# Performance work log

Hardware: AMD Instinct MI355X
Metric: run time of the kernel (lower is better)

## Reference

```python
import jax, jax.numpy as jnp
import numpy as np

KSIZE = 3   # patch kernel
NSIZE = 7   # search neighborhood
SCALE = 4   # downscale factor
ALPHA = 1


def _patches(x, k, pad_mode):
    # x: [b,c,h,w] -> [b, c*k*k, h, w], feature ordering channel-major
    # (matches torch.nn.functional.unfold ordering).
    if pad_mode == 'reflect':
        p = k // 2
        xp = jnp.pad(x, ((0, 0), (0, 0), (p, p), (p, p)), mode='reflect')
        return jax.lax.conv_general_dilated_patches(xp, (k, k), (1, 1), 'VALID')
    return jax.lax.conv_general_dilated_patches(x, (k, k), (1, 1), 'SAME')


def census(x):
    # UFlow-style soft census transform (the CensusTransform used in this repo):
    # grayscale*255, 3x3 zero-padded patches minus center, soft-sign normalize.
    gray = (0.299 * x[:, 0:1] + 0.587 * x[:, 1:2] + 0.114 * x[:, 2:3]) * 255.0
    p = _patches(gray, KSIZE, 'zero')          # [b, 9, h, w]
    t = p - gray
    return t / jnp.sqrt(0.81 + t * t)


def downsample(x):
    b, c, h, w = x.shape
    return jax.image.resize(x, (b, c, h // SCALE, w // SCALE), method='cubic')


def unfold_center(x):
    # _unfold(data, with_unfold=False): [b,c,h,w] -> [b, hw, c*k*k]
    x = downsample(x)
    b, c, h, w = x.shape
    p = _patches(x, KSIZE, 'reflect').reshape(b, c * KSIZE * KSIZE, h * w)
    return p.transpose(0, 2, 1)


def unfold_nbr(x):
    # _unfold(data, with_unfold=True): [b,c,h,w] -> [b, hw, n*n, c*k*k]
    x = downsample(x)
    b, c, h, w = x.shape
    d1 = _patches(x, KSIZE, 'reflect')          # [b, c*k*k, h, w]
    c1 = d1.shape[1]
    d2 = _patches(d1, NSIZE, 'reflect')         # [b, c1*n*n, h, w]
    d2 = d2.reshape(b, c1, NSIZE * NSIZE, h * w)
    return d2.transpose(0, 3, 2, 1)


def reference(pred, I):
    # --- census-space distance + argmin over 2*n*n candidates ---
    p_ct = unfold_center(census(pred))                       # [b, hw, 81]
    nbr_ct = jnp.concatenate(
        [unfold_nbr(census(I[:, 0])), unfold_nbr(census(I[:, 1]))], axis=2
    )                                                        # [b, hw, 2n^2, 81]
    # ||p - n||^2 expanded as p2 + n2 - 2 p.n (avoids the huge repeated diff)
    p2 = jnp.sum(p_ct * p_ct, axis=-1)                       # [b, hw]
    n2 = jnp.sum(nbr_ct * nbr_ct, axis=-1)                   # [b, hw, 2n^2]
    dis = p2[:, :, None] + n2 - 2.0 * jnp.einsum('bpc,bpnc->bpn', p_ct, nbr_ct)
    ind = jnp.argmin(dis, axis=2)                            # [b, hw]
    # --- gather matched raw patches and compute loss ---
    p = unfold_center(pred)                                  # [b, hw, 27]
    nbr = jnp.concatenate(
        [unfold_nbr(I[:, 0]), unfold_nbr(I[:, 1])], axis=2
    )                                                        # [b, hw, 2n^2, 27]
    matched = jnp.take_along_axis(nbr, ind[:, :, None, None], axis=2)[:, :, 0]
    return jnp.mean((p - matched) ** 2 * 0.5)


def setup_inputs() -> dict:
    key = jax.random.key(0)
    k1, k2 = jax.random.split(key)
    pred = jax.random.normal(k1, (2, 3, 384, 384), dtype=jnp.float32)
    I = jax.random.normal(k2, (2, 2, 3, 384, 384), dtype=jnp.float32)
    return {'pred': pred, 'I': I}
```

## Files before the change

### kernel.cpp

```cpp
#include <hip/hip_runtime.h>
#include <math.h>

#define FH 384
#define FW 384
#define DH 96
#define DW 96
#define NIMG 6
#define PLANE (DH * DW)
#define NPIX (2 * PLANE)

__device__ __forceinline__ float keysc(float x) {
    if (x < 1.f) return ((1.5f * x - 2.5f) * x) * x + 1.f;
    if (x < 2.f) return ((-0.5f * x + 2.5f) * x - 4.f) * x + 2.f;
    return 0.f;
}

__device__ __forceinline__ int refl(int i, int n) {
    if (i < 0) i = -i;
    if (i >= n) i = 2 * (n - 1) - i;
    return i;
}

__global__ void k_gray(const float* __restrict__ pred, const float* __restrict__ I,
                       float* __restrict__ gray) {
    int idx = blockIdx.x * 256 + threadIdx.x;
    const int total = NIMG * FH * FW;
    if (idx >= total) return;
    int img = idx / (FH * FW);
    int px  = idx % (FH * FW);
    const float* src;
    if (img < 2) {
        src = pred + img * 3 * FH * FW;
    } else {
        int j = (img - 2) >> 1, b = (img - 2) & 1;
        src = I + ((b * 2 + j) * 3) * FH * FW;
    }
    float r = src[px], g = src[FH * FW + px], b = src[2 * FH * FW + px];
    gray[idx] = (0.299f * r + 0.587f * g + 0.114f * b) * 255.0f;
}

__global__ void k_field(const float* __restrict__ gray, float* __restrict__ CF) {
    int idx = blockIdx.x * 256 + threadIdx.x;
    const int total = NIMG * FH * FW;
    if (idx >= total) return;
    int x   = idx % FW;
    int t1  = idx / FW;
    int r   = t1 % FH;
    int img = t1 / FH;
    const float* g = gray + img * FH * FW;
    float gc = g[r * FW + x];
    const int planeF = FH * FW;
    float* out = CF + ((size_t)img * 8) * planeF + r * FW + x;
    int ck = 0;
#pragma unroll
    for (int k = 0; k < 9; ++k) {
        if (k == 4) continue;
        int dy = k / 3 - 1, dx = k % 3 - 1;
        int r2 = r + dy, c2 = x + dx;
        float gn = (r2 < 0 || r2 >= FH || c2 < 0 || c2 >= FW) ? 0.f : g[r2 * FW + c2];
        float tt = gn - gc;
        out[ck * planeF] = tt / sqrtf(0.81f + tt * tt);
        ++ck;
    }
}

__global__ void k_census_downH(const float* __restrict__ CF, float* __restrict__ CH) {
    int idx = blockIdx.x * 256 + threadIdx.x;
    const int total = NIMG * 9 * DH * FW;
    if (idx >= total) return;
    int x  = idx % FW;
    int t1 = idx / FW;
    int yo = t1 % DH;
    int t2 = t1 / DH;
    int k  = t2 % 9;
    int img = t2 / 9;
    if (k == 4) { CH[idx] = 0.f; return; }
    int ck = (k < 4) ? k : k - 1;
    const float* F = CF + ((size_t)(img * 8 + ck) * FH) * FW + x;
    int rbase = 4 * yo - 6;
    float acc = 0.f, z = 0.f;
    if (rbase >= 0 && rbase + 15 < FH) {
#pragma unroll
        for (int t = 0; t < 16; ++t) {
            float w = keysc(fabsf((float)t - 7.5f) * 0.25f);
            z += w;
            acc += w * F[(rbase + t) * FW];
        }
    } else {
#pragma unroll
        for (int t = 0; t < 16; ++t) {
            int r = rbase + t;
            if (r < 0 || r >= FH) continue;
            float w = keysc(fabsf((float)t - 7.5f) * 0.25f);
            z += w;
            acc += w * F[r * FW];
        }
    }
    CH[idx] = acc / z;
}

__global__ void k_downW(const float* __restrict__ src, float* __restrict__ dst, int nrows) {
    int idx = blockIdx.x * 256 + threadIdx.x;
    int total = nrows * DW;
    if (idx >= total) return;
    int xo = idx % DW;
    int row = idx / DW;
    const float* s = src + row * FW;
    float acc = 0.f, z = 0.f;
#pragma unroll
    for (int t = 0; t < 16; ++t) {
        int i = 4 * xo - 6 + t;
        if (i < 0 || i >= FW) continue;
        float w = keysc(fabsf((float)t - 7.5f) * 0.25f);
        z += w;
        acc += w * s[i];
    }
    dst[idx] = acc / z;
}

__global__ void k_raw_downH(const float* __restrict__ pred, const float* __restrict__ I,
                            float* __restrict__ RH) {
    int idx = blockIdx.x * 256 + threadIdx.x;
    const int total = NIMG * 3 * DH * FW;
    if (idx >= total) return;
    int x  = idx % FW;
    int t1 = idx / FW;
    int yo = t1 % DH;
    int t2 = t1 / DH;
    int c  = t2 % 3;
    int img = t2 / 3;
    const float* src;
    if (img < 2) {
        src = pred + (img * 3 + c) * FH * FW;
    } else {
        int j = (img - 2) >> 1, b = (img - 2) & 1;
        src = I + (((b * 2 + j) * 3) + c) * FH * FW;
    }
    float acc = 0.f, z = 0.f;
#pragma unroll
    for (int t = 0; t < 16; ++t) {
        int r = 4 * yo - 6 + t;
        if (r < 0 || r >= FH) continue;
        float w = keysc(fabsf((float)t - 7.5f) * 0.25f);
        z += w;
        acc += w * src[r * FW + x];
    }
    RH[idx] = acc / z;
}

__global__ void k_n2(const float* __restrict__ CD, float* __restrict__ N2) {
    int idx = blockIdx.x * 256 + threadIdx.x;
    if (idx >= 4 * PLANE) return;
    int img4 = idx / PLANE;
    int pos  = idx % PLANE;
    int y = pos / DW, x = pos % DW;
    int ry[3], rx[3];
#pragma unroll
    for (int kk = 0; kk < 3; ++kk) {
        ry[kk] = refl(y + kk - 1, DH);
        rx[kk] = refl(x + kk - 1, DW);
    }
    const float* C = CD + (2 + img4) * 9 * PLANE;
    float s = 0.f;
#pragma unroll
    for (int c = 0; c < 9; ++c)
#pragma unroll
        for (int ky = 0; ky < 3; ++ky)
#pragma unroll
            for (int kx = 0; kx < 3; ++kx) {
                float v = C[c * PLANE + ry[ky] * DW + rx[kx]];
                s += v * v;
            }
    N2[idx] = s;
}

__global__ __launch_bounds__(256) void k_match_int(const float* __restrict__ CD,
                                                   const float* __restrict__ N2,
                                                   float* __restrict__ bestd,
                                                   int* __restrict__ bestn) {
    int bid  = blockIdx.x;
    int g    = bid / 72;
    int tile = bid % 72;
    int pid  = tile * 256 + threadIdx.x;
    int j  = g / 7;
    int dy = g % 7 - 3;
    int b   = pid / PLANE;
    int pos = pid % PLANE;
    int y = pos / DW, x = pos % DW;

    int yy = refl(y + dy, DH);
    int r0 = refl(yy - 1, DH), r1 = yy, r2 = refl(yy + 1, DH);
    int pr0 = refl(y - 1, DH), pr2 = refl(y + 1, DH);
    int xb = min(max(x - 4, 0), DW - 9);
    int xp = min(max(x - 1, 0), DW - 3);

    const float* Cp  = CD + (b * 9) * PLANE;
    const float* Cn  = CD + ((2 + 2 * j + b) * 9) * PLANE;
    const float* N2p = N2 + (2 * j + b) * PLANE;

    float dot[7];
#pragma unroll
    for (int i = 0; i < 7; ++i) dot[i] = 0.f;

#pragma unroll
    for (int c = 0; c < 9; ++c) {
        const float* pc = Cp + c * PLANE;
        const float* nc = Cn + c * PLANE;
        float p0[3], p1[3], p2[3];
#pragma unroll
        for (int kx = 0; kx < 3; ++kx) {
            p0[kx] = pc[pr0 * DW + xp + kx];
            p1[kx] = pc[y   * DW + xp + kx];
            p2[kx] = pc[pr2 * DW + xp + kx];
        }
        float w0[9], w1[9], w2[9];
#pragma unroll
        for (int i = 0; i < 9; ++i) {
            w0[i] = nc[r0 * DW + xb + i];
            w1[i] = nc[r1 * DW + xb + i];
            w2[i] = nc[r2 * DW + xb + i];
        }
#pragma unroll
        for (int dx = 0; dx < 7; ++dx) {
            float d = dot[dx];
            d += p0[0] * w0[dx + 0]; d += p0[1] * w0[dx + 1]; d += p0[2] * w0[dx + 2];
            d += p1[0] * w1[dx + 0]; d += p1[1] * w1[dx + 1]; d += p1[2] * w1[dx + 2];
            d += p2[0] * w2[dx + 0]; d += p2[1] * w2[dx + 1]; d += p2[2] * w2[dx + 2];
            dot[dx] = d;
        }
    }

    float best = INFINITY;
    int bn = 1 << 30;
    int nbase = j * 49 + (dy + 3) * 7;
#pragma unroll
    for (int dx = 0; dx < 7; ++dx) {
        int xxc = min(max(x + dx - 3, 0), DW - 1);
        float dis = N2p[yy * DW + xxc] - 2.f * dot[dx];
        if (dis < best) { best = dis; bn = nbase + dx; }
    }
    bestd[g * NPIX + pid] = best;
    bestn[g * NPIX + pid] = bn;
}

__global__ __launch_bounds__(256) void k_match_edge(const float* __restrict__ CD,
                                                    const float* __restrict__ N2,
                                                    float* __restrict__ bestd,
                                                    int* __restrict__ bestn) {
    __shared__ float part[4][64];
    __shared__ float disw[4][8];

    int wid  = threadIdx.x >> 6;
    int lane = threadIdx.x & 63;
    int item = blockIdx.x * 4 + wid;
    int g  = item / 1536;
    int pe = item % 1536;
    int j = g / 7, dy = g % 7 - 3;
    int b   = pe / 768;
    int rem = pe % 768;
    int y  = rem / 8;
    int xi = rem % 8;
    int x  = (xi < 4) ? xi : 88 + xi;
    int pid = b * PLANE + y * DW + x;
    int yy = refl(y + dy, DH);

    int c = lane / 7, dx = lane % 7;
    float partial = 0.f;
    if (lane < 63) {
        int xx = refl(x + dx - 3, DW);
        const float* pc = CD + (b * 9 + c) * PLANE;
        const float* nc = CD + ((2 + 2 * j + b) * 9 + c) * PLANE;
#pragma unroll
        for (int ky = 0; ky < 3; ++ky) {
            int pry = refl(y + ky - 1, DH);
            int nry = refl(yy + ky - 1, DH);
#pragma unroll
            for (int kx = 0; kx < 3; ++kx) {
                int prx = refl(x + kx - 1, DW);
                int nrx = refl(xx + kx - 1, DW);
                partial += pc[pry * DW + prx] * nc[nry * DW + nrx];
            }
        }
    }
    part[wid][lane] = partial;
    __syncthreads();

    if (lane < 7) {
        float dot = 0.f;
#pragma unroll
        for (int cc = 0; cc < 9; ++cc) dot += part[wid][cc * 7 + lane];
        int xxl = refl(x + lane - 3, DW);
        disw[wid][lane] = N2[(2 * j + b) * PLANE + yy * DW + xxl] - 2.f * dot;
    }
    __syncthreads();

    if (lane == 0) {
        float best = INFINITY;
        int bn = 1 << 30;
        int nbase = j * 49 + (dy + 3) * 7;
#pragma unroll
        for (int dxx = 0; dxx < 7; ++dxx) {
            float d = disw[wid][dxx];
            if (d < best) { best = d; bn = nbase + dxx; }
        }
        bestd[g * NPIX + pid] = best;
        bestn[g * NPIX + pid] = bn;
    }
}

__global__ __launch_bounds__(256) void k_combine(const float* __restrict__ bestd,
                                                 const int* __restrict__ bestn,
                                                 const float* __restrict__ RD,
                                                 float* __restrict__ partial) {
    int pid = blockIdx.x * 256 + threadIdx.x;
    int b   = pid / PLANE;
    int pos = pid % PLANE;
    int y = pos / DW, x = pos % DW;

    float d0 = bestd[pid];
    int   n0 = bestn[pid];
#pragma unroll
    for (int g = 1; g < 14; ++g) {
        float d = bestd[g * NPIX + pid];
        int   n = bestn[g * NPIX + pid];
        if (d < d0 || (d == d0 && n < n0)) { d0 = d; n0 = n; }
    }

    int j = n0 / 49, rr = n0 % 49;
    int dy = rr / 7 - 3, dx = rr % 7 - 3;
    int yy = refl(y + dy, DH), xx = refl(x + dx, DW);
    int ry0[3], rx0[3], ry[3], rx[3];
#pragma unroll
    for (int kk = 0; kk < 3; ++kk) {
        ry0[kk] = refl(y + kk - 1, DH);
        rx0[kk] = refl(x + kk - 1, DW);
        ry[kk]  = refl(yy + kk - 1, DH);
        rx[kk]  = refl(xx + kk - 1, DW);
    }
    const float* RDp = RD + b * 3 * PLANE;
    const float* RDn = RD + (2 + 2 * j + b) * 3 * PLANE;
    float loss = 0.f;
#pragma unroll
    for (int c = 0; c < 3; ++c)
#pragma unroll
        for (int ky = 0; ky < 3; ++ky)
#pragma unroll
            for (int kx = 0; kx < 3; ++kx) {
                float a = RDp[c * PLANE + ry0[ky] * DW + rx0[kx]];
                float m = RDn[c * PLANE + ry[ky] * DW + rx[kx]];
                float d = a - m;
                loss += d * d;
            }

    __shared__ float red[256];
    red[threadIdx.x] = loss;
    __syncthreads();
#pragma unroll
    for (int s = 128; s > 0; s >>= 1) {
        if (threadIdx.x < s) red[threadIdx.x] += red[threadIdx.x + s];
        __syncthreads();
    }
    if (threadIdx.x == 0) partial[blockIdx.x] = red[0];
}

#define NPART 72
__global__ void k_final(const float* __restrict__ partial, float* __restrict__ out) {
    __shared__ float red[128];
    float v = (threadIdx.x < NPART) ? partial[threadIdx.x] : 0.f;
    red[threadIdx.x] = v;
    __syncthreads();
#pragma unroll
    for (int s = 64; s > 0; s >>= 1) {
        if (threadIdx.x < s) red[threadIdx.x] += red[threadIdx.x + s];
        __syncthreads();
    }
    if (threadIdx.x == 0) out[0] = red[0] * (0.5f / 497664.0f);
}

extern "C" void kernel_launch(void* const* d_in, const int* in_sizes, int n_in,
                              void* d_out, int out_size, void* d_ws, size_t ws_size,
                              hipStream_t stream) {
    const float* pred = (const float*)d_in[0];
    const float* I    = (const float*)d_in[1];
    float* out = (float*)d_out;
    float* ws  = (float*)d_ws;

    float* CD   = ws;
    float* RD   = CD + 497664;
    float* S    = RD + 165888;
    float* gray = S;
    float* CF   = S + 884736;
    float* CH   = S + 7962624;
    float* RH   = S + 9953280;
    float* N2   = S;
    float* bestd = S + 36864;
    int*   bestn = (int*)(S + 294912);
    float* part  = S + 552960;

    k_gray<<<(NIMG * FH * FW + 255) / 256, 256, 0, stream>>>(pred, I, gray);
    k_field<<<(NIMG * FH * FW + 255) / 256, 256, 0, stream>>>(gray, CF);
    k_census_downH<<<(NIMG * 9 * DH * FW + 255) / 256, 256, 0, stream>>>(CF, CH);
    k_raw_downH<<<(NIMG * 3 * DH * FW + 255) / 256, 256, 0, stream>>>(pred, I, RH);
    k_downW<<<((NIMG * 12 * DH) * DW + 255) / 256, 256, 0, stream>>>(CH, CD, NIMG * 12 * DH);
    k_n2<<<(4 * PLANE + 255) / 256, 256, 0, stream>>>(CD, N2);
    k_match_int<<<14 * 72, 256, 0, stream>>>(CD, N2, bestd, bestn);
    k_match_edge<<<(14 * 1536) / 4 / 64, 256, 0, stream>>>(CD, N2, bestd, bestn);
    k_combine<<<NPIX / 256, 256, 0, stream>>>(bestd, bestn, RD, part);
    k_final<<<1, 128, 0, stream>>>(part, out);
}
```

Before: 116.2 us.

## Fuse gray into census field, merge downH kernels with float4, merge match kernels

Computes grayscale on the fly inside the census-field kernel, which removes the separate gray pass and its buffer. The census and raw vertical downsampling kernels are merged into one launch that processes four columns per thread with float4 loads. The interior and edge matching kernels become a single launch, and interior threads now skip writing border columns that the edge path owns. This cuts launch count and intermediate traffic, at the cost of recomputing gray up to nine times per pixel and adding a branchy fused kernel.

Result: slower. 147.9 us (+27.3%).

```diff
diff --git a/kernel.cpp b/kernel.cpp
--- a/kernel.cpp
+++ b/kernel.cpp
@@ -21,25 +21,8 @@
     return i;
 }
 
-__global__ void k_gray(const float* __restrict__ pred, const float* __restrict__ I,
-                       float* __restrict__ gray) {
-    int idx = blockIdx.x * 256 + threadIdx.x;
-    const int total = NIMG * FH * FW;
-    if (idx >= total) return;
-    int img = idx / (FH * FW);
-    int px  = idx % (FH * FW);
-    const float* src;
-    if (img < 2) {
-        src = pred + img * 3 * FH * FW;
-    } else {
-        int j = (img - 2) >> 1, b = (img - 2) & 1;
-        src = I + ((b * 2 + j) * 3) * FH * FW;
-    }
-    float r = src[px], g = src[FH * FW + px], b = src[2 * FH * FW + px];
-    gray[idx] = (0.299f * r + 0.587f * g + 0.114f * b) * 255.0f;
-}
-
-__global__ void k_field(const float* __restrict__ gray, float* __restrict__ CF) {
+__global__ void k_field(const float* __restrict__ pred, const float* __restrict__ I,
+                        float* __restrict__ CF) {
     int idx = blockIdx.x * 256 + threadIdx.x;
     const int total = NIMG * FH * FW;
     if (idx >= total) return;
@@ -47,9 +30,19 @@
     int t1  = idx / FW;
     int r   = t1 % FH;
     int img = t1 / FH;
-    const float* g = gray + img * FH * FW;
-    float gc = g[r * FW + x];
+    const float* src;
+    if (img < 2) {
+        src = pred + img * 3 * FH * FW;
+    } else {
+        int j = (img - 2) >> 1, b = (img - 2) & 1;
+        src = I + ((b * 2 + j) * 3) * FH * FW;
+    }
     const int planeF = FH * FW;
+    auto grayAt = [&](int rr, int cc) -> float {
+        const float* s = src + rr * FW + cc;
+        return (0.299f * s[0] + 0.587f * s[planeF] + 0.114f * s[2 * planeF]) * 255.0f;
+    };
+    float gc = grayAt(r, x);
     float* out = CF + ((size_t)img * 8) * planeF + r * FW + x;
     int ck = 0;
 #pragma unroll
@@ -57,34 +50,75 @@
         if (k == 4) continue;
         int dy = k / 3 - 1, dx = k % 3 - 1;
         int r2 = r + dy, c2 = x + dx;
-        float gn = (r2 < 0 || r2 >= FH || c2 < 0 || c2 >= FW) ? 0.f : g[r2 * FW + c2];
+        float gn = (r2 < 0 || r2 >= FH || c2 < 0 || c2 >= FW) ? 0.f : grayAt(r2, c2);
         float tt = gn - gc;
         out[ck * planeF] = tt / sqrtf(0.81f + tt * tt);
         ++ck;
     }
 }
 
-__global__ void k_census_downH(const float* __restrict__ CF, float* __restrict__ CH) {
+#define CTOT (NIMG * 9 * DH * (FW / 4))
+#define RTOT (NIMG * 3 * DH * (FW / 4))
+__global__ void k_downH(const float* __restrict__ CF, const float* __restrict__ pred,
+                        const float* __restrict__ I, float* __restrict__ CH,
+                        float* __restrict__ RH) {
     int idx = blockIdx.x * 256 + threadIdx.x;
-    const int total = NIMG * 9 * DH * FW;
-    if (idx >= total) return;
-    int x  = idx % FW;
-    int t1 = idx / FW;
-    int yo = t1 % DH;
-    int t2 = t1 / DH;
-    int k  = t2 % 9;
-    int img = t2 / 9;
-    if (k == 4) { CH[idx] = 0.f; return; }
-    int ck = (k < 4) ? k : k - 1;
-    const float* F = CF + ((size_t)(img * 8 + ck) * FH) * FW + x;
+    if (idx >= CTOT + RTOT) return;
+    const int planeF = FH * FW;
+
+    const float4* F;
+    float4* outp;
+    int yo;
+    bool zero_out = false;
+    if (idx < CTOT) {
+        int x4 = idx % 96;
+        int t1 = idx / 96;
+        yo     = t1 % DH;
+        int t2 = t1 / DH;
+        int k  = t2 % 9;
+        int img = t2 / 9;
+        outp = (float4*)CH + idx;
+        if (k == 4) {
+            zero_out = true;
+            F = (const float4*)CF;
+        } else {
+            int ck = (k < 4) ? k : k - 1;
+            F = (const float4*)(CF + (size_t)(img * 8 + ck) * planeF) + x4;
+        }
+    } else {
+        int rid = idx - CTOT;
+        int x4 = rid % 96;
+        int t1 = rid / 96;
+        yo     = t1 % DH;
+        int t2 = t1 / DH;
+        int c  = t2 % 3;
+        int img = t2 / 3;
+        const float* src;
+        if (img < 2) {
+            src = pred + (img * 3 + c) * planeF;
+        } else {
+            int j = (img - 2) >> 1, b = (img - 2) & 1;
+            src = I + (((b * 2 + j) * 3) + c) * planeF;
+        }
+        F = (const float4*)src + x4;
+        outp = (float4*)RH + rid;
+    }
+
+    if (zero_out) {
+        *outp = make_float4(0.f, 0.f, 0.f, 0.f);
+        return;
+    }
+
     int rbase = 4 * yo - 6;
-    float acc = 0.f, z = 0.f;
+    float4 acc = make_float4(0.f, 0.f, 0.f, 0.f);
+    float z = 0.f;
     if (rbase >= 0 && rbase + 15 < FH) {
 #pragma unroll
         for (int t = 0; t < 16; ++t) {
             float w = keysc(fabsf((float)t - 7.5f) * 0.25f);
             z += w;
-            acc += w * F[(rbase + t) * FW];
+            float4 v = F[(rbase + t) * 96];
+            acc.x += w * v.x; acc.y += w * v.y; acc.z += w * v.z; acc.w += w * v.w;
         }
     } else {
 #pragma unroll
@@ -93,10 +127,11 @@
             if (r < 0 || r >= FH) continue;
             float w = keysc(fabsf((float)t - 7.5f) * 0.25f);
             z += w;
-            acc += w * F[r * FW];
-        }
-    }
-    CH[idx] = acc / z;
+            float4 v = F[r * 96];
+            acc.x += w * v.x; acc.y += w * v.y; acc.z += w * v.z; acc.w += w * v.w;
+        }
+    }
+    *outp = make_float4(acc.x / z, acc.y / z, acc.z / z, acc.w / z);
 }
 
 __global__ void k_downW(const float* __restrict__ src, float* __restrict__ dst, int nrows) {
@@ -118,36 +153,6 @@
     dst[idx] = acc / z;
 }
 
-__global__ void k_raw_downH(const float* __restrict__ pred, const float* __restrict__ I,
-                            float* __restrict__ RH) {
-    int idx = blockIdx.x * 256 + threadIdx.x;
-    const int total = NIMG * 3 * DH * FW;
-    if (idx >= total) return;
-    int x  = idx % FW;
-    int t1 = idx / FW;
-    int yo = t1 % DH;
-    int t2 = t1 / DH;
-    int c  = t2 % 3;
-    int img = t2 / 3;
-    const float* src;
-    if (img < 2) {
-        src = pred + (img * 3 + c) * FH * FW;
-    } else {
-        int j = (img - 2) >> 1, b = (img - 2) & 1;
-        src = I + (((b * 2 + j) * 3) + c) * FH * FW;
-    }
-    float acc = 0.f, z = 0.f;
-#pragma unroll
-    for (int t = 0; t < 16; ++t) {
-        int r = 4 * yo - 6 + t;
-        if (r < 0 || r >= FH) continue;
-        float w = keysc(fabsf((float)t - 7.5f) * 0.25f);
-        z += w;
-        acc += w * src[r * FW + x];
-    }
-    RH[idx] = acc / z;
-}
-
 __global__ void k_n2(const float* __restrict__ CD, float* __restrict__ N2) {
     int idx = blockIdx.x * 256 + threadIdx.x;
     if (idx >= 4 * PLANE) return;
@@ -174,137 +179,139 @@
     N2[idx] = s;
 }
 
-__global__ __launch_bounds__(256) void k_match_int(const float* __restrict__ CD,
-                                                   const float* __restrict__ N2,
-                                                   float* __restrict__ bestd,
-                                                   int* __restrict__ bestn) {
-    int bid  = blockIdx.x;
-    int g    = bid / 72;
-    int tile = bid % 72;
-    int pid  = tile * 256 + threadIdx.x;
-    int j  = g / 7;
-    int dy = g % 7 - 3;
-    int b   = pid / PLANE;
-    int pos = pid % PLANE;
-    int y = pos / DW, x = pos % DW;
-
-    int yy = refl(y + dy, DH);
-    int r0 = refl(yy - 1, DH), r1 = yy, r2 = refl(yy + 1, DH);
-    int pr0 = refl(y - 1, DH), pr2 = refl(y + 1, DH);
-    int xb = min(max(x - 4, 0), DW - 9);
-    int xp = min(max(x - 1, 0), DW - 3);
-
-    const float* Cp  = CD + (b * 9) * PLANE;
-    const float* Cn  = CD + ((2 + 2 * j + b) * 9) * PLANE;
-    const float* N2p = N2 + (2 * j + b) * PLANE;
-
-    float dot[7];
-#pragma unroll
-    for (int i = 0; i < 7; ++i) dot[i] = 0.f;
-
-#pragma unroll
-    for (int c = 0; c < 9; ++c) {
-        const float* pc = Cp + c * PLANE;
-        const float* nc = Cn + c * PLANE;
-        float p0[3], p1[3], p2[3];
-#pragma unroll
-        for (int kx = 0; kx < 3; ++kx) {
-            p0[kx] = pc[pr0 * DW + xp + kx];
-            p1[kx] = pc[y   * DW + xp + kx];
-            p2[kx] = pc[pr2 * DW + xp + kx];
-        }
-        float w0[9], w1[9], w2[9];
-#pragma unroll
-        for (int i = 0; i < 9; ++i) {
-            w0[i] = nc[r0 * DW + xb + i];
-            w1[i] = nc[r1 * DW + xb + i];
-            w2[i] = nc[r2 * DW + xb + i];
-        }
-#pragma unroll
-        for (int dx = 0; dx < 7; ++dx) {
-            float d = dot[dx];
-            d += p0[0] * w0[dx + 0]; d += p0[1] * w0[dx + 1]; d += p0[2] * w0[dx + 2];
-            d += p1[0] * w1[dx + 0]; d += p1[1] * w1[dx + 1]; d += p1[2] * w1[dx + 2];
-            d += p2[0] * w2[dx + 0]; d += p2[1] * w2[dx + 1]; d += p2[2] * w2[dx + 2];
-            dot[dx] = d;
-        }
-    }
-
-    float best = INFINITY;
-    int bn = 1 << 30;
-    int nbase = j * 49 + (dy + 3) * 7;
-#pragma unroll
-    for (int dx = 0; dx < 7; ++dx) {
-        int xxc = min(max(x + dx - 3, 0), DW - 1);
-        float dis = N2p[yy * DW + xxc] - 2.f * dot[dx];
-        if (dis < best) { best = dis; bn = nbase + dx; }
-    }
-    bestd[g * NPIX + pid] = best;
-    bestn[g * NPIX + pid] = bn;
-}
-
-__global__ __launch_bounds__(256) void k_match_edge(const float* __restrict__ CD,
-                                                    const float* __restrict__ N2,
-                                                    float* __restrict__ bestd,
-                                                    int* __restrict__ bestn) {
+#define NINT_BLK (14 * 72)
+#define NEDGE_ITEMS (14 * 1536)
+#define NEDGE_BLK (NEDGE_ITEMS / 4)
+__global__ __launch_bounds__(256) void k_match(const float* __restrict__ CD,
+                                               const float* __restrict__ N2,
+                                               float* __restrict__ bestd,
+                                               int* __restrict__ bestn) {
     __shared__ float part[4][64];
     __shared__ float disw[4][8];
 
-    int wid  = threadIdx.x >> 6;
-    int lane = threadIdx.x & 63;
-    int item = blockIdx.x * 4 + wid;
-    int g  = item / 1536;
-    int pe = item % 1536;
-    int j = g / 7, dy = g % 7 - 3;
-    int b   = pe / 768;
-    int rem = pe % 768;
-    int y  = rem / 8;
-    int xi = rem % 8;
-    int x  = (xi < 4) ? xi : 88 + xi;
-    int pid = b * PLANE + y * DW + x;
-    int yy = refl(y + dy, DH);
-
-    int c = lane / 7, dx = lane % 7;
-    float partial = 0.f;
-    if (lane < 63) {
-        int xx = refl(x + dx - 3, DW);
-        const float* pc = CD + (b * 9 + c) * PLANE;
-        const float* nc = CD + ((2 + 2 * j + b) * 9 + c) * PLANE;
-#pragma unroll
-        for (int ky = 0; ky < 3; ++ky) {
-            int pry = refl(y + ky - 1, DH);
-            int nry = refl(yy + ky - 1, DH);
+    if (blockIdx.x < NINT_BLK) {
+        int bid  = blockIdx.x;
+        int g    = bid / 72;
+        int tile = bid % 72;
+        int pid  = tile * 256 + threadIdx.x;
+        int j  = g / 7;
+        int dy = g % 7 - 3;
+        int b   = pid / PLANE;
+        int pos = pid % PLANE;
+        int y = pos / DW, x = pos % DW;
+
+        int yy = refl(y + dy, DH);
+        int r0 = refl(yy - 1, DH), r1 = yy, r2 = refl(yy + 1, DH);
+        int pr0 = refl(y - 1, DH), pr2 = refl(y + 1, DH);
+        int xb = min(max(x - 4, 0), DW - 9);
+        int xp = min(max(x - 1, 0), DW - 3);
+
+        const float* Cp  = CD + (b * 9) * PLANE;
+        const float* Cn  = CD + ((2 + 2 * j + b) * 9) * PLANE;
+        const float* N2p = N2 + (2 * j + b) * PLANE;
+
+        float dot[7];
+#pragma unroll
+        for (int i = 0; i < 7; ++i) dot[i] = 0.f;
+
+#pragma unroll
+        for (int c = 0; c < 9; ++c) {
+            const float* pc = Cp + c * PLANE;
+            const float* nc = Cn + c * PLANE;
+            float p0[3], p1[3], p2[3];
 #pragma unroll
             for (int kx = 0; kx < 3; ++kx) {
-                int prx = refl(x + kx - 1, DW);
-                int nrx = refl(xx + kx - 1, DW);
-                partial += pc[pry * DW + prx] * nc[nry * DW + nrx];
-            }
-        }
-    }
-    part[wid][lane] = partial;
-    __syncthreads();
-
-    if (lane < 7) {
-        float dot = 0.f;
-#pragma unroll
-        for (int cc = 0; cc < 9; ++cc) dot += part[wid][cc * 7 + lane];
-        int xxl = refl(x + lane - 3, DW);
-        disw[wid][lane] = N2[(2 * j + b) * PLANE + yy * DW + xxl] - 2.f * dot;
-    }
-    __syncthreads();
-
-    if (lane == 0) {
+                p0[kx] = pc[pr0 * DW + xp + kx];
+                p1[kx] = pc[y   * DW + xp + kx];
+                p2[kx] = pc[pr2 * DW + xp + kx];
+            }
+            float w0[9], w1[9], w2[9];
+#pragma unroll
+            for (int i = 0; i < 9; ++i) {
+                w0[i] = nc[r0 * DW + xb + i];
+                w1[i] = nc[r1 * DW + xb + i];
+                w2[i] = nc[r2 * DW + xb + i];
+            }
+#pragma unroll
+            for (int dx = 0; dx < 7; ++dx) {
+                float d = dot[dx];
+                d += p0[0] * w0[dx + 0]; d += p0[1] * w0[dx + 1]; d += p0[2] * w0[dx + 2];
+                d += p1[0] * w1[dx + 0]; d += p1[1] * w1[dx + 1]; d += p1[2] * w1[dx + 2];
+                d += p2[0] * w2[dx + 0]; d += p2[1] * w2[dx + 1]; d += p2[2] * w2[dx + 2];
+                dot[dx] = d;
+            }
+        }
+
         float best = INFINITY;
         int bn = 1 << 30;
         int nbase = j * 49 + (dy + 3) * 7;
 #pragma unroll
-        for (int dxx = 0; dxx < 7; ++dxx) {
-            float d = disw[wid][dxx];
-            if (d < best) { best = d; bn = nbase + dxx; }
-        }
-        bestd[g * NPIX + pid] = best;
-        bestn[g * NPIX + pid] = bn;
+        for (int dx = 0; dx < 7; ++dx) {
+            int xxc = min(max(x + dx - 3, 0), DW - 1);
+            float dis = N2p[yy * DW + xxc] - 2.f * dot[dx];
+            if (dis < best) { best = dis; bn = nbase + dx; }
+        }
+        if (x >= 4 && x < 92) {
+            bestd[g * NPIX + pid] = best;
+            bestn[g * NPIX + pid] = bn;
+        }
+    } else {
+        int wid  = threadIdx.x >> 6;
+        int lane = threadIdx.x & 63;
+        int item = (blockIdx.x - NINT_BLK) * 4 + wid;
+        int g  = item / 1536;
+        int pe = item % 1536;
+        int j = g / 7, dy = g % 7 - 3;
+        int b   = pe / 768;
+        int rem = pe % 768;
+        int y  = rem / 8;
+        int xi = rem % 8;
+        int x  = (xi < 4) ? xi : 88 + xi;
+        int pid = b * PLANE + y * DW + x;
+        int yy = refl(y + dy, DH);
+
+        int c = lane / 7, dx = lane % 7;
+        float partial = 0.f;
+        if (lane < 63) {
+            int xx = refl(x + dx - 3, DW);
+            const float* pc = CD + (b * 9 + c) * PLANE;
+            const float* nc = CD + ((2 + 2 * j + b) * 9 + c) * PLANE;
+#pragma unroll
+            for (int ky = 0; ky < 3; ++ky) {
+                int pry = refl(y + ky - 1, DH);
+                int nry = refl(yy + ky - 1, DH);
+#pragma unroll
+                for (int kx = 0; kx < 3; ++kx) {
+                    int prx = refl(x + kx - 1, DW);
+                    int nrx = refl(xx + kx - 1, DW);
+                    partial += pc[pry * DW + prx] * nc[nry * DW + nrx];
+                }
+            }
+        }
+        part[wid][lane] = partial;
+        __syncthreads();
+
+        if (lane < 7) {
+            float dot = 0.f;
+#pragma unroll
+            for (int cc = 0; cc < 9; ++cc) dot += part[wid][cc * 7 + lane];
+            int xxl = refl(x + lane - 3, DW);
+            disw[wid][lane] = N2[(2 * j + b) * PLANE + yy * DW + xxl] - 2.f * dot;
+        }
+        __syncthreads();
+
+        if (lane == 0) {
+            float best = INFINITY;
+            int bn = 1 << 30;
+            int nbase = j * 49 + (dy + 3) * 7;
+#pragma unroll
+            for (int dxx = 0; dxx < 7; ++dxx) {
+                float d = disw[wid][dxx];
+                if (d < best) { best = d; bn = nbase + dxx; }
+            }
+            bestd[g * NPIX + pid] = best;
+            bestn[g * NPIX + pid] = bn;
+        }
     }
 }
 
@@ -388,23 +395,19 @@
     float* CD   = ws;
     float* RD   = CD + 497664;
     float* S    = RD + 165888;
-    float* gray = S;
-    float* CF   = S + 884736;
-    float* CH   = S + 7962624;
-    float* RH   = S + 9953280;
+    float* CF   = S;
+    float* CH   = S + 7077888;
+    float* RH   = S + 9068544;
     float* N2   = S;
     float* bestd = S + 36864;
     int*   bestn = (int*)(S + 294912);
     float* part  = S + 552960;
 
-    k_gray<<<(NIMG * FH * FW + 255) / 256, 256, 0, stream>>>(pred, I, gray);
-    k_field<<<(NIMG * FH * FW + 255) / 256, 256, 0, stream>>>(gray, CF);
-    k_census_downH<<<(NIMG * 9 * DH * FW + 255) / 256, 256, 0, stream>>>(CF, CH);
-    k_raw_downH<<<(NIMG * 3 * DH * FW + 255) / 256, 256, 0, stream>>>(pred, I, RH);
+    k_field<<<(NIMG * FH * FW + 255) / 256, 256, 0, stream>>>(pred, I, CF);
+    k_downH<<<(CTOT + RTOT + 255) / 256, 256, 0, stream>>>(CF, pred, I, CH, RH);
     k_downW<<<((NIMG * 12 * DH) * DW + 255) / 256, 256, 0, stream>>>(CH, CD, NIMG * 12 * DH);
     k_n2<<<(4 * PLANE + 255) / 256, 256, 0, stream>>>(CD, N2);
-    k_match_int<<<14 * 72, 256, 0, stream>>>(CD, N2, bestd, bestn);
-    k_match_edge<<<(14 * 1536) / 4 / 64, 256, 0, stream>>>(CD, N2, bestd, bestn);
+    k_match<<<NINT_BLK + NEDGE_BLK, 256, 0, stream>>>(CD, N2, bestd, bestn);
     k_combine<<<NPIX / 256, 256, 0, stream>>>(bestd, bestn, RD, part);
     k_final<<<1, 128, 0, stream>>>(part, out);
 }
```
